# Performance work log

Hardware: AMD Instinct MI355X
Metric: run time of the kernel (lower is better)

The kernel has to match this reference:

```python
import jax, jax.numpy as jnp
import numpy as np


def setup_inputs() -> dict:
    key = jax.random.key(0)
    k1, k2, k3, k4, k5 = jax.random.split(key, 5)
    B, T, N, F, H = 32, 12, 512, 64, 64
    cat_x = jax.random.normal(k1, (B, T, N, F), dtype=jnp.float32)
    # Linear params (stored as [in, out]; torch stores [out, in] and does x @ W.T)
    lim = 1.0 / np.sqrt(F)
    Wq = jax.random.uniform(k2, (F, H), jnp.float32, -lim, lim)
    bq = jax.random.uniform(k3, (H,), jnp.float32, -lim, lim)
    Wk = jax.random.uniform(k4, (F, H), jnp.float32, -lim, lim)
    bk = jax.random.uniform(k5, (H,), jnp.float32, -lim, lim)
    return {"cat_x": cat_x, "Wq": Wq, "bq": bq, "Wk": Wk, "bk": bk, "tau": 4}


def reference(cat_x, Wq, bq, Wk, bk, tau):
    # cat_x: [B, T, N, F]
    q = cat_x @ Wq + bq  # [B, T, N, H]
    k = cat_x @ Wk + bk  # [B, T, N, H]
    qf = jnp.fft.rfft(q, axis=-1)  # [B, T, N, Fr]
    kf = jnp.fft.rfft(k, axis=-1)  # [B, T, N, Fr]
    # Vectorized over the original Python loop over i (query time step):
    # res[b, i, j, n, :] = qf[b, i, n, :] * conj(kf[b, j, n, :])
    res = qf[:, :, None, :, :] * jnp.conj(kf)[:, None, :, :, :]  # [B, Ti, Tj, N, Fr]
    corr = jnp.fft.irfft(res, axis=-1)  # [B, Ti, Tj, N, H] (H even -> exact round trip)
    # mean over batch, then hidden (last), then nodes == mean over (B, N, H)
    score_set = jnp.mean(corr, axis=(0, 3, 4))  # [Ti, Tj]
    scores, indices = jax.lax.top_k(score_set, tau)
    return scores, indices
```

## Files before the change

### kernel.cpp

```cpp
#include <hip/hip_runtime.h>

#define BB 32
#define TT 12
#define NN 512
#define FF 64
#define HH 64
#define NBLK 8
#define NCHUNK (NN / NBLK)
#define GRID (BB * NCHUNK)
#define NSHADOW 16

#define WS_SH 0
#define WS_WQ (NSHADOW * TT * TT)
#define WS_WK (WS_WQ + FF)
#define WS_BQ (WS_WK + FF)
#define WS_BK (WS_BQ + 1)

__global__ __launch_bounds__(1024) void fft_sel_init(
    const float* __restrict__ Wq, const float* __restrict__ bq,
    const float* __restrict__ Wk, const float* __restrict__ bk,
    float* __restrict__ ws)
{
    const int tid = threadIdx.x;
    if (tid < 576) {
        ((float4*)ws)[tid] = make_float4(0.f, 0.f, 0.f, 0.f);
    } else if (tid < 576 + FF) {
        const int f = tid - 576;
        float a = 0.f;
        #pragma unroll
        for (int h = 0; h < HH; ++h) a += Wq[f * HH + h];
        ws[WS_WQ + f] = a;
    } else if (tid < 576 + 2 * FF) {
        const int f = tid - (576 + FF);
        float a = 0.f;
        #pragma unroll
        for (int h = 0; h < HH; ++h) a += Wk[f * HH + h];
        ws[WS_WK + f] = a;
    } else if (tid == 576 + 2 * FF) {
        float a = 0.f;
        #pragma unroll
        for (int h = 0; h < HH; ++h) a += bq[h];
        ws[WS_BQ] = a;
    } else if (tid == 576 + 2 * FF + 1) {
        float a = 0.f;
        #pragma unroll
        for (int h = 0; h < HH; ++h) a += bk[h];
        ws[WS_BK] = a;
    }
}

__global__ __launch_bounds__(256, 8) void fft_sel_main(
    const float* __restrict__ x,
    const float* __restrict__ ws)
{
    __shared__ float sq[TT][NBLK];
    __shared__ float sk[TT][NBLK];

    const int tid = threadIdx.x;
    const int q   = tid & 15;

    const float4 wqv = *(const float4*)(ws + WS_WQ + 4 * q);
    const float4 wkv = *(const float4*)(ws + WS_WK + 4 * q);
    const float  bqs = ws[WS_BQ];
    const float  bks = ws[WS_BK];

    const int b  = blockIdx.x >> 6;
    const int n0 = (blockIdx.x & (NCHUNK - 1)) * NBLK;

    #pragma unroll
    for (int it = 0; it < (TT * NBLK * 16) / 256; ++it) {
        const int s   = it * 256 + tid;
        const int row = s >> 4;
        const int t   = row >> 3;
        const int nl  = row & (NBLK - 1);
        const float4 v = *(const float4*)(x +
            (((size_t)b * TT + t) * NN + (n0 + nl)) * FF + q * 4);
        float pq = v.x * wqv.x + v.y * wqv.y + v.z * wqv.z + v.w * wqv.w;
        float pk = v.x * wkv.x + v.y * wkv.y + v.z * wkv.z + v.w * wkv.w;
        #pragma unroll
        for (int off = 1; off < 16; off <<= 1) {
            pq += __shfl_xor(pq, off);
            pk += __shfl_xor(pk, off);
        }
        if (q == 0) {
            sq[t][nl] = pq + bqs;
            sk[t][nl] = pk + bks;
        }
    }
    __syncthreads();

    if (tid < TT * TT) {
        const int i = tid / TT;
        const int j = tid % TT;
        float acc = 0.f;
        #pragma unroll
        for (int nl = 0; nl < NBLK; ++nl) acc += sq[i][nl] * sk[j][nl];
        float* S = (float*)ws + WS_SH + (blockIdx.x & (NSHADOW - 1)) * (TT * TT);
        atomicAdd(&S[tid], acc);
    }
}

__global__ __launch_bounds__(256) void fft_sel_final(
    const float* __restrict__ ws, float* __restrict__ out)
{
    __shared__ float S[TT * TT];
    const int tid = threadIdx.x;
    if (tid < TT * TT) {
        const float scale = 1.0f / ((float)BB * (float)NN * (float)HH);
        float a = 0.f;
        #pragma unroll
        for (int c = 0; c < NSHADOW; ++c) a += ws[WS_SH + c * TT * TT + tid];
        S[tid] = a * scale;
    }
    __syncthreads();
    if (tid < TT) {
        const int i = tid;
        float v[TT];
        bool used[TT];
        #pragma unroll
        for (int j = 0; j < TT; ++j) { v[j] = S[i * TT + j]; used[j] = false; }
        #pragma unroll
        for (int s = 0; s < 4; ++s) {
            float best = -INFINITY;
            int bi = 0;
            for (int j = 0; j < TT; ++j) {
                if (!used[j] && v[j] > best) { best = v[j]; bi = j; }
            }
            used[bi] = true;
            out[i * 4 + s]          = best;
            out[TT * 4 + i * 4 + s] = (float)bi;
        }
    }
}

extern "C" void kernel_launch(void* const* d_in, const int* in_sizes, int n_in,
                              void* d_out, int out_size, void* d_ws, size_t ws_size,
                              hipStream_t stream) {
    const float* x  = (const float*)d_in[0];
    const float* Wq = (const float*)d_in[1];
    const float* bq = (const float*)d_in[2];
    const float* Wk = (const float*)d_in[3];
    const float* bk = (const float*)d_in[4];
    float* ws = (float*)d_ws;

    fft_sel_init<<<1, 1024, 0, stream>>>(Wq, bq, Wk, bk, ws);
    fft_sel_main<<<GRID, 256, 0, stream>>>(x, ws);
    fft_sel_final<<<1, 256, 0, stream>>>(ws, (float*)d_out);
}
```

Baseline: 97.72 us.

## Fuse weight-sum init into main kernel and replace atomics with per-block partials

Drops the separate init kernel: each main block recomputes the column sums of Wq/Wk and the bias sums into shared memory. The shadow-buffer atomics are replaced by writing every block's 144 partial dot products to a [144][GRID] buffer. The final kernel now runs one block per query row and reduces those partials with wave-level shuffles before the top-k. This removes one launch and the atomic contention, at the cost of redundant weight reads in every block and a larger partial buffer for the final pass to read.

```diff
diff --git a/kernel.cpp b/kernel.cpp
--- a/kernel.cpp
+++ b/kernel.cpp
@@ -8,61 +8,52 @@
 #define NBLK 8
 #define NCHUNK (NN / NBLK)
 #define GRID (BB * NCHUNK)
-#define NSHADOW 16
 
-#define WS_SH 0
-#define WS_WQ (NSHADOW * TT * TT)
-#define WS_WK (WS_WQ + FF)
-#define WS_BQ (WS_WK + FF)
-#define WS_BK (WS_BQ + 1)
-
-__global__ __launch_bounds__(1024) void fft_sel_init(
-    const float* __restrict__ Wq, const float* __restrict__ bq,
-    const float* __restrict__ Wk, const float* __restrict__ bk,
-    float* __restrict__ ws)
-{
-    const int tid = threadIdx.x;
-    if (tid < 576) {
-        ((float4*)ws)[tid] = make_float4(0.f, 0.f, 0.f, 0.f);
-    } else if (tid < 576 + FF) {
-        const int f = tid - 576;
-        float a = 0.f;
-        #pragma unroll
-        for (int h = 0; h < HH; ++h) a += Wq[f * HH + h];
-        ws[WS_WQ + f] = a;
-    } else if (tid < 576 + 2 * FF) {
-        const int f = tid - (576 + FF);
-        float a = 0.f;
-        #pragma unroll
-        for (int h = 0; h < HH; ++h) a += Wk[f * HH + h];
-        ws[WS_WK + f] = a;
-    } else if (tid == 576 + 2 * FF) {
-        float a = 0.f;
-        #pragma unroll
-        for (int h = 0; h < HH; ++h) a += bq[h];
-        ws[WS_BQ] = a;
-    } else if (tid == 576 + 2 * FF + 1) {
-        float a = 0.f;
-        #pragma unroll
-        for (int h = 0; h < HH; ++h) a += bk[h];
-        ws[WS_BK] = a;
-    }
-}
 
 __global__ __launch_bounds__(256, 8) void fft_sel_main(
     const float* __restrict__ x,
-    const float* __restrict__ ws)
+    const float* __restrict__ Wq, const float* __restrict__ bq,
+    const float* __restrict__ Wk, const float* __restrict__ bk,
+    float* __restrict__ P)
 {
+    __shared__ __align__(16) float wq_s[FF];
+    __shared__ __align__(16) float wk_s[FF];
+    __shared__ float bsum[2];
     __shared__ float sq[TT][NBLK];
     __shared__ float sk[TT][NBLK];
 
     const int tid = threadIdx.x;
-    const int q   = tid & 15;
 
-    const float4 wqv = *(const float4*)(ws + WS_WQ + 4 * q);
-    const float4 wkv = *(const float4*)(ws + WS_WK + 4 * q);
-    const float  bqs = ws[WS_BQ];
-    const float  bks = ws[WS_BK];
+    if (tid < FF) {
+        const float* p = Wq + tid * HH;
+        float a = 0.f;
+        #pragma unroll
+        for (int h = 0; h < HH; ++h) a += p[h];
+        wq_s[tid] = a;
+    } else if (tid < 2 * FF) {
+        const float* p = Wk + (tid - FF) * HH;
+        float a = 0.f;
+        #pragma unroll
+        for (int h = 0; h < HH; ++h) a += p[h];
+        wk_s[tid - FF] = a;
+    } else if (tid == 2 * FF) {
+        float a = 0.f;
+        #pragma unroll
+        for (int h = 0; h < HH; ++h) a += bq[h];
+        bsum[0] = a;
+    } else if (tid == 2 * FF + 1) {
+        float a = 0.f;
+        #pragma unroll
+        for (int h = 0; h < HH; ++h) a += bk[h];
+        bsum[1] = a;
+    }
+    __syncthreads();
+
+    const int q = tid & 15;
+    const float4 wqv = *(const float4*)(wq_s + 4 * q);
+    const float4 wkv = *(const float4*)(wk_s + 4 * q);
+    const float  bqs = bsum[0];
+    const float  bks = bsum[1];
 
     const int b  = blockIdx.x >> 6;
     const int n0 = (blockIdx.x & (NCHUNK - 1)) * NBLK;
@@ -95,40 +86,50 @@
         float acc = 0.f;
         #pragma unroll
         for (int nl = 0; nl < NBLK; ++nl) acc += sq[i][nl] * sk[j][nl];
-        float* S = (float*)ws + WS_SH + (blockIdx.x & (NSHADOW - 1)) * (TT * TT);
-        atomicAdd(&S[tid], acc);
+        P[(size_t)tid * GRID + blockIdx.x] = acc;
     }
 }
 
 __global__ __launch_bounds__(256) void fft_sel_final(
-    const float* __restrict__ ws, float* __restrict__ out)
+    const float* __restrict__ P, float* __restrict__ out)
 {
-    __shared__ float S[TT * TT];
-    const int tid = threadIdx.x;
-    if (tid < TT * TT) {
-        const float scale = 1.0f / ((float)BB * (float)NN * (float)HH);
-        float a = 0.f;
+    __shared__ float S[TT];
+    const int i    = blockIdx.x;
+    const int wave = threadIdx.x >> 6;
+    const int lane = threadIdx.x & 63;
+
+    #pragma unroll
+    for (int jj = 0; jj < 3; ++jj) {
+        const int j = wave + 4 * jj;
+        const float* row = P + (size_t)(i * TT + j) * GRID;
+        float s = 0.f;
         #pragma unroll
-        for (int c = 0; c < NSHADOW; ++c) a += ws[WS_SH + c * TT * TT + tid];
-        S[tid] = a * scale;
+        for (int k = 0; k < GRID / 256; ++k) {
+            const float4 a = *(const float4*)(row + k * 256 + lane * 4);
+            s += a.x + a.y + a.z + a.w;
+        }
+        #pragma unroll
+        for (int off = 1; off < 64; off <<= 1) s += __shfl_xor(s, off);
+        if (lane == 0) S[j] = s;
     }
     __syncthreads();
-    if (tid < TT) {
-        const int i = tid;
+
+    if (threadIdx.x == 0) {
+        const float scale = 1.0f / ((float)BB * (float)NN * (float)HH);
         float v[TT];
         bool used[TT];
         #pragma unroll
-        for (int j = 0; j < TT; ++j) { v[j] = S[i * TT + j]; used[j] = false; }
+        for (int j = 0; j < TT; ++j) { v[j] = S[j] * scale; used[j] = false; }
         #pragma unroll
-        for (int s = 0; s < 4; ++s) {
+        for (int s4 = 0; s4 < 4; ++s4) {
             float best = -INFINITY;
             int bi = 0;
             for (int j = 0; j < TT; ++j) {
                 if (!used[j] && v[j] > best) { best = v[j]; bi = j; }
             }
             used[bi] = true;
-            out[i * 4 + s]          = best;
-            out[TT * 4 + i * 4 + s] = (float)bi;
+            out[i * 4 + s4]          = best;
+            out[TT * 4 + i * 4 + s4] = (float)bi;
         }
     }
 }
@@ -141,9 +142,8 @@
     const float* bq = (const float*)d_in[2];
     const float* Wk = (const float*)d_in[3];
     const float* bk = (const float*)d_in[4];
-    float* ws = (float*)d_ws;
+    float* P = (float*)d_ws;
 
-    fft_sel_init<<<1, 1024, 0, stream>>>(Wq, bq, Wk, bk, ws);
-    fft_sel_main<<<GRID, 256, 0, stream>>>(x, ws);
-    fft_sel_final<<<1, 256, 0, stream>>>(ws, (float*)d_out);
+    fft_sel_main<<<GRID, 256, 0, stream>>>(x, Wq, bq, Wk, bk, P);
+    fft_sel_final<<<TT, 256, 0, stream>>>(P, (float*)d_out);
 }
```

New measurement: 103.3 us. 5.7% more time.
